# Optimization experiments

Hardware: AMD Instinct MI355X
Metric: run time of the kernel (lower is better)

## Reference

```python
import jax, jax.numpy as jnp
import numpy as np

NEG_SLOPE = 0.2
LN_EPS = 1e-5


def _layernorm(x, g, b):
    mu = jnp.mean(x, axis=-1, keepdims=True)
    var = jnp.mean(jnp.square(x - mu), axis=-1, keepdims=True)
    return (x - mu) * jax.lax.rsqrt(var + LN_EPS) * g + b


def _gat_layer(x, src, dst, ew, W, al, ar, bias, resW, act):
    # x: [N, F_in], W: [F_in, H*D], al/ar: [H, D], bias: [H*D]
    N = x.shape[0]
    H, D = al.shape
    feat = (x @ W).reshape(N, H, D)
    el = jnp.einsum('nhd,hd->nh', feat, al)          # [N, H]
    er = jnp.einsum('nhd,hd->nh', feat, ar)          # [N, H]
    e = jax.nn.leaky_relu(el[src] + er[dst], NEG_SLOPE)  # [E, H]
    # segment softmax over incoming edges of each destination node
    emax = jax.ops.segment_max(e, dst, num_segments=N)
    emax = jnp.where(jnp.isfinite(emax), emax, 0.0)
    ex = jnp.exp(e - emax[dst])
    den = jax.ops.segment_sum(ex, dst, num_segments=N)
    a = ex / den[dst] * ew[:, None]                  # [E, H] (edge_weight scales post-softmax, DGL semantics)
    msg = feat[src] * a[:, :, None]                  # [E, H, D]
    rst = jax.ops.segment_sum(msg, dst, num_segments=N)  # [N, H, D]
    res = (x @ resW).reshape(N, H, D) if resW is not None else x.reshape(N, H, D)
    rst = rst + res + bias.reshape(1, H, D)
    if act is not None:
        rst = act(rst)
    return rst.reshape(N, H * D)


def setup_inputs() -> dict:
    key = jax.random.key(0)
    ks = jax.random.split(key, 24)
    N, E, F_in, H, D = 100000, 1600000, 256, 4, 32
    HD = H * D
    s = 0.1
    inp = {
        'x': jax.random.normal(ks[0], (N, F_in), jnp.float32),
        'src': jax.random.randint(ks[1], (E,), 0, N, jnp.int32),
        'dst': jax.random.randint(ks[2], (E,), 0, N, jnp.int32),
        'edge_weight': jax.random.uniform(ks[3], (E,), jnp.float32),
        # layer 0: in 256 -> 4 heads x 32, residual Linear
        'W0': jax.random.normal(ks[4], (F_in, HD), jnp.float32) * s,
        'al0': jax.random.normal(ks[5], (H, D), jnp.float32) * s,
        'ar0': jax.random.normal(ks[6], (H, D), jnp.float32) * s,
        'b0': jnp.zeros((HD,), jnp.float32),
        'resW0': jax.random.normal(ks[7], (F_in, HD), jnp.float32) * s,
        'ln0_g': jnp.ones((HD,), jnp.float32),
        'ln0_b': jnp.zeros((HD,), jnp.float32),
        # layer 1: 128 -> 4x32, identity residual
        'W1': jax.random.normal(ks[8], (HD, HD), jnp.float32) * s,
        'al1': jax.random.normal(ks[9], (H, D), jnp.float32) * s,
        'ar1': jax.random.normal(ks[10], (H, D), jnp.float32) * s,
        'b1': jnp.zeros((HD,), jnp.float32),
        'ln1_g': jnp.ones((HD,), jnp.float32),
        'ln1_b': jnp.zeros((HD,), jnp.float32),
        # layer 2 (last, no activation)
        'W2': jax.random.normal(ks[11], (HD, HD), jnp.float32) * s,
        'al2': jax.random.normal(ks[12], (H, D), jnp.float32) * s,
        'ar2': jax.random.normal(ks[13], (H, D), jnp.float32) * s,
        'b2': jnp.zeros((HD,), jnp.float32),
        'ln2_g': jnp.ones((HD,), jnp.float32),
        'ln2_b': jnp.zeros((HD,), jnp.float32),
    }
    return inp


def reference(x, src, dst, edge_weight,
              W0, al0, ar0, b0, resW0, ln0_g, ln0_b,
              W1, al1, ar1, b1, ln1_g, ln1_b,
              W2, al2, ar2, b2, ln2_g, ln2_b):
    h = _gat_layer(x, src, dst, edge_weight, W0, al0, ar0, b0, resW0, jax.nn.elu)
    h = _layernorm(h, ln0_g, ln0_b)
    h = _gat_layer(h, src, dst, edge_weight, W1, al1, ar1, b1, None, jax.nn.elu)
    h = _layernorm(h, ln1_g, ln1_b)
    h = _gat_layer(h, src, dst, edge_weight, W2, al2, ar2, b2, None, None)
    h = _layernorm(h, ln2_g, ln2_b)
    return h
```

## Files before the change

kernel.cpp:

```cpp
#include <hip/hip_runtime.h>
#include <hip/hip_bf16.h>
#include <hip/hip_fp16.h>
#include <math.h>

#define DEV __device__ __forceinline__

typedef short v8s __attribute__((ext_vector_type(8)));
typedef float v4f __attribute__((ext_vector_type(4)));
typedef __fp16 fp16x2 __attribute__((ext_vector_type(2)));

DEV float bf2f(unsigned short u) {
    union { unsigned int i; float f; } c; c.i = ((unsigned int)u) << 16; return c.f;
}
DEV unsigned short f2bf(float f) {
    union { float f; unsigned int u; } c; c.f = f;
    unsigned int u = c.u;
    unsigned int r = u + 0x7fffu + ((u >> 16) & 1u);
    return (unsigned short)(r >> 16);
}
DEV unsigned short f2h(float f) {
    union { _Float16 h; unsigned short u; } c; c.h = (_Float16)f; return c.u;
}
DEV float h2f(unsigned short u) {
    union { unsigned short u; _Float16 h; } c; c.u = u; return (float)c.h;
}
DEV unsigned int pkdup(float x) {
    union { fp16x2 h; unsigned int u; } c;
    c.h = __builtin_amdgcn_cvt_pkrtz(x, x);
    return c.u;
}
DEV __half2 bitcast_h2(unsigned int u) {
    union { unsigned int u; __half2 h; } c; c.u = u; return c.h;
}

#if __has_builtin(__builtin_amdgcn_exp2f)
DEV float fexp2(float x) { return __builtin_amdgcn_exp2f(x); }
#else
DEV float fexp2(float x) { float r; asm("v_exp_f32 %0, %1" : "=v"(r) : "v"(x)); return r; }
#endif
#if __has_builtin(__builtin_amdgcn_rcpf)
DEV float frcp(float x) { return __builtin_amdgcn_rcpf(x); }
#else
DEV float frcp(float x) { float r; asm("v_rcp_f32 %0, %1" : "=v"(r) : "v"(x)); return r; }
#endif
#if __has_builtin(__builtin_amdgcn_rsqf)
DEV float frsq(float x) { return __builtin_amdgcn_rsqf(x); }
#else
DEV float frsq(float x) { float r; asm("v_rsq_f32 %0, %1" : "=v"(r) : "v"(x)); return r; }
#endif
DEV unsigned int cvtpk_bf16(float lo, float hi) {
    unsigned int r;
    asm("v_cvt_pk_bf16_f32 %0, %1, %2" : "=v"(r) : "v"(lo), "v"(hi));
    return r;
}

__global__ void detect_kernel(const unsigned short* __restrict__ w, int* __restrict__ flag) {
    __shared__ int cnt;
    if (threadIdx.x == 0) cnt = 0;
    __syncthreads();
    int c = 0;
    for (int i = threadIdx.x; i < 2048; i += 256) {
        unsigned short u = w[i * 2];
        int e = (u >> 7) & 0xff;
        if (e >= 110 && e <= 132) c++;
    }
    atomicAdd(&cnt, c);
    __syncthreads();
    if (threadIdx.x == 0) *flag = (cnt > 1024) ? 1 : 0;
}


__global__ void zero_kernel(int* __restrict__ p, int n) {
    int i = blockIdx.x * 256 + threadIdx.x;
    if (i < n) p[i] = 0;
}

__global__ void degree_kernel(const int* __restrict__ dst, int* __restrict__ deg, int E) {
    int i = blockIdx.x * 256 + threadIdx.x;
    if (i < E) atomicAdd(&deg[dst[i]], 1);
}

__global__ __launch_bounds__(1024)
void scan_kernel(const int* __restrict__ deg, int* __restrict__ rowptr, int n) {
    __shared__ int wtot[16];
    const int tid  = threadIdx.x;
    const int lane = tid & 63;
    const int wid  = tid >> 6;
    int carry = 0;
    for (int base = 0; base < n; base += 4096) {
        int i0 = base + tid * 4;
        int v0 = (i0     < n) ? deg[i0]     : 0;
        int v1 = (i0 + 1 < n) ? deg[i0 + 1] : 0;
        int v2 = (i0 + 2 < n) ? deg[i0 + 2] : 0;
        int v3 = (i0 + 3 < n) ? deg[i0 + 3] : 0;
        int s = v0 + v1 + v2 + v3;
        int sc = s;
        #pragma unroll
        for (int d = 1; d < 64; d <<= 1) {
            int t = __shfl_up(sc, d);
            if (lane >= d) sc += t;
        }
        if (lane == 63) wtot[wid] = sc;
        __syncthreads();
        int woff = 0, tot = 0;
        #pragma unroll
        for (int w = 0; w < 16; ++w) {
            int t = wtot[w];
            if (w < wid) woff += t;
            tot += t;
        }
        int p = carry + woff + (sc - s);
        if (i0     < n) rowptr[i0]     = p; p += v0;
        if (i0 + 1 < n) rowptr[i0 + 1] = p; p += v1;
        if (i0 + 2 < n) rowptr[i0 + 2] = p; p += v2;
        if (i0 + 3 < n) rowptr[i0 + 3] = p;
        carry += tot;
        __syncthreads();
    }
    if (tid == 0) rowptr[n] = carry;
}

__global__ void scatter_kernel(const int* __restrict__ src, const int* __restrict__ dst,
                               const void* __restrict__ ew, const int* __restrict__ flagp,
                               const int* __restrict__ rowptr, int* __restrict__ cur,
                               int2* __restrict__ csr, int E) {
    int i = blockIdx.x * 256 + threadIdx.x;
    if (i < E) {
        int isbf = *flagp;
        int d = dst[i];
        int pos = atomicAdd(&cur[d], 1);
        int slot = rowptr[d] + pos;
        float wv = isbf ? bf2f(((const unsigned short*)ew)[i]) : ((const float*)ew)[i];
        csr[slot] = make_int2(src[i], __float_as_int(wv));
    }
}

__global__ void convx_kernel(const void* __restrict__ x, unsigned short* __restrict__ xbf,
                             const int* __restrict__ flagp, long n8) {
    if (*flagp) return;
    long i = ((long)blockIdx.x * 256 + threadIdx.x) * 8;
    if (i >= n8 * 8) return;
    const float* xf = (const float*)x + i;
    unsigned int o[4];
    #pragma unroll
    for (int j = 0; j < 4; ++j)
        o[j] = cvtpk_bf16(xf[j*2], xf[j*2+1]);
    *(uint4*)(xbf + i) = make_uint4(o[0], o[1], o[2], o[3]);
}

__global__ void wtrans_kernel(const void* __restrict__ B, unsigned short* __restrict__ Btp,
                              const int* __restrict__ flagp, int K) {
    int i = blockIdx.x * 256 + threadIdx.x;
    if (i >= 128 * K) return;
    int j = i & 7;
    int l = (i >> 3) & 63;
    int t = (i >> 9) & 7;
    int c = i >> 12;
    int k = c * 32 + ((l >> 4) * 8) + j;
    int n = t * 16 + (l & 15);
    unsigned short v;
    if (*flagp) v = ((const unsigned short*)B)[k * 128 + n];
    else        v = f2bf(((const float*)B)[k * 128 + n]);
    Btp[i] = v;
}

__global__ __launch_bounds__(256)
void gemm_mfma(const unsigned short* __restrict__ Aext, const unsigned short* __restrict__ Aconv,
               const int* __restrict__ flagp,
               const unsigned short* __restrict__ Btp,
               unsigned short* __restrict__ Cout, int M, int K, int out_half) {
    const unsigned short* A = (*flagp) ? Aext : Aconv;
    const int lane = threadIdx.x & 63;
    const int wid  = threadIdx.x >> 6;
    const long tile = (long)blockIdx.x * 4 + wid;
    const long m0 = tile * 16;
    if (m0 >= M) return;
    const int r = lane & 15, quad = lane >> 4;
    long arow = m0 + r; if (arow >= M) arow = M - 1;
    const unsigned short* ap = A + arow * K + quad * 8;
    v4f acc[8];
    #pragma unroll
    for (int t = 0; t < 8; ++t) acc[t] = (v4f){0.f, 0.f, 0.f, 0.f};
    for (int k0 = 0; k0 < K; k0 += 32) {
        v8s af = *(const v8s*)(ap + k0);
        const unsigned short* bp = Btp + ((size_t)(k0 >> 5) * 8) * 512 + lane * 8;
        #pragma unroll
        for (int t = 0; t < 8; ++t) {
            v8s bf = *(const v8s*)(bp + t * 512);
            acc[t] = __builtin_amdgcn_mfma_f32_16x16x32_bf16(af, bf, acc[t], 0, 0, 0);
        }
    }
    if (out_half) {
        #pragma unroll
        for (int t = 0; t < 8; ++t) {
            const int col = t * 16 + r;
            #pragma unroll
            for (int reg = 0; reg < 4; ++reg) {
                long grow = m0 + quad * 4 + reg;
                if (grow < M) Cout[grow * 128 + col] = f2h(acc[t][reg]);
            }
        }
    } else {
        #pragma unroll
        for (int t = 0; t < 8; t += 2) {
            const int col0 = t * 16 + r, col1 = (t + 1) * 16 + r;
            #pragma unroll
            for (int reg = 0; reg < 4; ++reg) {
                long grow = m0 + quad * 4 + reg;
                unsigned int pk = cvtpk_bf16(acc[t][reg], acc[t + 1][reg]);
                if (grow < M) {
                    Cout[grow * 128 + col0] = (unsigned short)pk;
                    Cout[grow * 128 + col1] = (unsigned short)(pk >> 16);
                }
            }
        }
    }
}

__global__ __launch_bounds__(256)
void elr_kernel(const unsigned short* __restrict__ feath,
                const void* __restrict__ al, const void* __restrict__ ar,
                const int* __restrict__ flagp,
                float* __restrict__ el, float* __restrict__ er, int N) {
    int idx = blockIdx.x * 256 + threadIdx.x;
    if (idx >= N * 4) return;
    const int isbf = *flagp;
    int n = idx >> 2, h = idx & 3;
    const unsigned short* fr = feath + (long)n * 128 + h * 32;
    float av[32], bv[32];
    if (isbf) {
        const unsigned short* alp = (const unsigned short*)al + h * 32;
        const unsigned short* arp = (const unsigned short*)ar + h * 32;
        #pragma unroll
        for (int i = 0; i < 32; ++i) { av[i] = bf2f(alp[i]); bv[i] = bf2f(arp[i]); }
    } else {
        const float* alp = (const float*)al + h * 32;
        const float* arp = (const float*)ar + h * 32;
        #pragma unroll
        for (int i = 0; i < 32; ++i) { av[i] = alp[i]; bv[i] = arp[i]; }
    }
    float sl = 0.f, sr = 0.f;
    #pragma unroll
    for (int i = 0; i < 32; i += 8) {
        uint4 u = *(const uint4*)&fr[i];
        float f[8];
        f[0] = h2f((unsigned short)(u.x & 0xffffu)); f[1] = h2f((unsigned short)(u.x >> 16));
        f[2] = h2f((unsigned short)(u.y & 0xffffu)); f[3] = h2f((unsigned short)(u.y >> 16));
        f[4] = h2f((unsigned short)(u.z & 0xffffu)); f[5] = h2f((unsigned short)(u.z >> 16));
        f[6] = h2f((unsigned short)(u.w & 0xffffu)); f[7] = h2f((unsigned short)(u.w >> 16));
        #pragma unroll
        for (int j = 0; j < 8; ++j) { sl += f[j] * av[i + j]; sr += f[j] * bv[i + j]; }
    }
    el[idx] = sl; er[idx] = sr;
}


__global__ __launch_bounds__(256)
void aggregate_kernel(const unsigned short* __restrict__ feath,
                      const float4* __restrict__ el4,
                      const float4* __restrict__ er4,
                      const unsigned short* __restrict__ res_bf,
                      const void* __restrict__ bias,
                      const void* __restrict__ lng,
                      const void* __restrict__ lnb,
                      const int* __restrict__ flagp,
                      const int* __restrict__ rowptr,
                      const int2* __restrict__ csr,
                      unsigned short* __restrict__ out_bf,
                      float* __restrict__ out_f32,
                      int N, int apply_elu, int final_mode) {
    __shared__ int          s_src[4][64];
    __shared__ unsigned int s_pw[4][256];
    const int lane = threadIdx.x & 63;
    const int wid  = threadIdx.x >> 6;
    const int v = blockIdx.x * 4 + wid;
    if (v >= N) return;
    const int isbf = *flagp;
    const int eg = lane >> 4;
    const int fl = lane & 15;
    const int hd = fl >> 2;
    const int fb = fl * 8;
    const int p0 = rowptr[v], p1 = rowptr[v + 1];
    const float4 erv = er4[v];

    float den0 = 0.f, den1 = 0.f, den2 = 0.f, den3 = 0.f;
    __half2 acch[4];
    acch[0] = acch[1] = acch[2] = acch[3] = __float2half2_rn(0.f);

    for (int eb = p0; eb < p1; eb += 64) {
        const int cnt = min(64, p1 - eb);
        int s = 0;
        unsigned int pw0 = 0, pw1 = 0, pw2 = 0, pw3 = 0;
        if (lane < cnt) {
            int2 sw = csr[eb + lane];
            s = sw.x;
            float w = __int_as_float(sw.y);
            float4 elv = el4[s];
            float t, q;
            t = elv.x + erv.x; t = fmaxf(t, 0.2f * t);
            q = fexp2(fmaf(t, 1.44269504f, -6.0f)); den0 += q; pw0 = pkdup(q * w);
            t = elv.y + erv.y; t = fmaxf(t, 0.2f * t);
            q = fexp2(fmaf(t, 1.44269504f, -6.0f)); den1 += q; pw1 = pkdup(q * w);
            t = elv.z + erv.z; t = fmaxf(t, 0.2f * t);
            q = fexp2(fmaf(t, 1.44269504f, -6.0f)); den2 += q; pw2 = pkdup(q * w);
            t = elv.w + erv.w; t = fmaxf(t, 0.2f * t);
            q = fexp2(fmaf(t, 1.44269504f, -6.0f)); den3 += q; pw3 = pkdup(q * w);
        }
        s_src[wid][lane] = s;
        *(uint4*)&s_pw[wid][lane * 4] = make_uint4(pw0, pw1, pw2, pw3);
        const int cntr = (cnt + 3) & ~3;
        for (int e = 0; e < cntr; e += 4) {
            int ee = e + eg;
            int se = s_src[wid][ee];
            __half2 ae = bitcast_h2(s_pw[wid][ee * 4 + hd]);
            uint4 u = *(const uint4*)(feath + (size_t)se * 128 + fb);
            acch[0] = __hfma2(ae, bitcast_h2(u.x), acch[0]);
            acch[1] = __hfma2(ae, bitcast_h2(u.y), acch[1]);
            acch[2] = __hfma2(ae, bitcast_h2(u.z), acch[2]);
            acch[3] = __hfma2(ae, bitcast_h2(u.w), acch[3]);
        }
    }
    #pragma unroll
    for (int j = 0; j < 4; ++j) {
        union { __half2 h; int i; } a;
        union { int i; __half2 h; } b;
        a.h = acch[j]; b.i = __shfl_xor(a.i, 16); acch[j] = __hadd2(acch[j], b.h);
        a.h = acch[j]; b.i = __shfl_xor(a.i, 32); acch[j] = __hadd2(acch[j], b.h);
    }
    #pragma unroll
    for (int d = 1; d < 64; d <<= 1) {
        den0 += __shfl_xor(den0, d);
        den1 += __shfl_xor(den1, d);
        den2 += __shfl_xor(den2, d);
        den3 += __shfl_xor(den3, d);
    }
    float den = (hd == 0) ? den0 : (hd == 1) ? den1 : (hd == 2) ? den2 : den3;
    float invd = (p1 > p0) ? frcp(den) : 0.f;
    float acc[8];
    #pragma unroll
    for (int j = 0; j < 4; ++j) {
        acc[j * 2]     = __low2float(acch[j]);
        acc[j * 2 + 1] = __high2float(acch[j]);
    }
    uint4 ru = *(const uint4*)(res_bf + (size_t)v * 128 + fb);
    float rv[8];
    rv[0] = bf2f((unsigned short)(ru.x & 0xffffu)); rv[1] = bf2f((unsigned short)(ru.x >> 16));
    rv[2] = bf2f((unsigned short)(ru.y & 0xffffu)); rv[3] = bf2f((unsigned short)(ru.y >> 16));
    rv[4] = bf2f((unsigned short)(ru.z & 0xffffu)); rv[5] = bf2f((unsigned short)(ru.z >> 16));
    rv[6] = bf2f((unsigned short)(ru.w & 0xffffu)); rv[7] = bf2f((unsigned short)(ru.w >> 16));
    float bsv[8], gv[8], lbv[8];
    if (isbf) {
        const unsigned short* bsp = (const unsigned short*)bias + fb;
        const unsigned short* gp  = (const unsigned short*)lng + fb;
        const unsigned short* bp  = (const unsigned short*)lnb + fb;
        #pragma unroll
        for (int j = 0; j < 8; ++j) { bsv[j] = bf2f(bsp[j]); gv[j] = bf2f(gp[j]); lbv[j] = bf2f(bp[j]); }
    } else {
        const float* bsp = (const float*)bias + fb;
        const float* gp  = (const float*)lng + fb;
        const float* bp  = (const float*)lnb + fb;
        #pragma unroll
        for (int j = 0; j < 8; ++j) { bsv[j] = bsp[j]; gv[j] = gp[j]; lbv[j] = bp[j]; }
    }
    float o[8];
    float ssum = 0.f;
    #pragma unroll
    for (int j = 0; j < 8; ++j) {
        float t = acc[j] * invd + rv[j] + bsv[j];
        if (apply_elu) t = (t > 0.f) ? t : fexp2(t * 1.44269504f) - 1.0f;
        o[j] = t;
        ssum += t;
    }
    #pragma unroll
    for (int d = 1; d < 16; d <<= 1) ssum += __shfl_xor(ssum, d);
    float mu = ssum * (1.0f / 128.0f);
    float vsum = 0.f;
    #pragma unroll
    for (int j = 0; j < 8; ++j) { float dd = o[j] - mu; vsum += dd * dd; }
    #pragma unroll
    for (int d = 1; d < 16; d <<= 1) vsum += __shfl_xor(vsum, d);
    float rs = frsq(vsum * (1.0f / 128.0f) + 1e-5f);
    if (eg == 0) {
        if (final_mode && !isbf) {
            float* op = out_f32 + (size_t)v * 128 + fb;
            #pragma unroll
            for (int j = 0; j < 8; ++j) op[j] = (o[j] - mu) * rs * gv[j] + lbv[j];
        } else {
            unsigned int w[4];
            #pragma unroll
            for (int j = 0; j < 4; ++j) {
                float lo = (o[j*2]   - mu) * rs * gv[j*2]   + lbv[j*2];
                float hi = (o[j*2+1] - mu) * rs * gv[j*2+1] + lbv[j*2+1];
                w[j] = cvtpk_bf16(lo, hi);
            }
            *(uint4*)(out_bf + (size_t)v * 128 + fb) = make_uint4(w[0], w[1], w[2], w[3]);
        }
    }
}


extern "C" void kernel_launch(void* const* d_in, const int* in_sizes, int n_in,
                              void* d_out, int out_size, void* d_ws, size_t ws_size,
                              hipStream_t stream) {
    const void* x    = d_in[0];
    const int* src   = (const int*)d_in[1];
    const int* dst   = (const int*)d_in[2];
    const void* ew   = d_in[3];
    const void* W0   = d_in[4];
    const void* al0  = d_in[5];
    const void* ar0  = d_in[6];
    const void* b0   = d_in[7];
    const void* resW0= d_in[8];
    const void* ln0g = d_in[9];
    const void* ln0b = d_in[10];
    const void* W1   = d_in[11];
    const void* al1  = d_in[12];
    const void* ar1  = d_in[13];
    const void* b1   = d_in[14];
    const void* ln1g = d_in[15];
    const void* ln1b = d_in[16];
    const void* W2   = d_in[17];
    const void* al2  = d_in[18];
    const void* ar2  = d_in[19];
    const void* b2   = d_in[20];
    const void* ln2g = d_in[21];
    const void* ln2b = d_in[22];

    const int HD  = 128;
    const int Fin = in_sizes[4] / HD;
    const int N   = in_sizes[0] / Fin;
    const int E   = in_sizes[1];

    char* ws = (char*)d_ws;
    size_t off = 0;
    auto alloc = [&](size_t bytes) -> void* {
        void* p = ws + off;
        off = (off + bytes + 255) & ~(size_t)255;
        return p;
    };
    int*   flag    = (int*)alloc(256);
    unsigned short* xbf   = (unsigned short*)alloc((size_t)N * Fin * 2);
    unsigned short* feat  = (unsigned short*)alloc((size_t)N * 128 * 2);
    unsigned short* h_bf  = (unsigned short*)alloc((size_t)N * 128 * 2);
    unsigned short* res0  = (unsigned short*)alloc((size_t)N * 128 * 2);
    float* el      = (float*)alloc((size_t)N * 4 * 4);
    float* er      = (float*)alloc((size_t)N * 4 * 4);
    int*   rowptr  = (int*)alloc((size_t)(N + 1) * 4);
    int*   deg     = (int*)alloc((size_t)N * 4);
    int*   cur     = (int*)alloc((size_t)N * 4);
    int2*  csr     = (int2*)alloc((size_t)E * 8);
    unsigned short* Bt0  = (unsigned short*)alloc((size_t)128 * Fin * 2);
    unsigned short* Btr0 = (unsigned short*)alloc((size_t)128 * Fin * 2);
    unsigned short* Bt1  = (unsigned short*)alloc((size_t)128 * HD * 2);
    unsigned short* Bt2  = (unsigned short*)alloc((size_t)128 * HD * 2);

    const int zb = (N + 255) / 256;
    const int eb = (E + 255) / 256;
    const int gblocks = (N + 63) / 64;
    const int ablocks = (N + 3) / 4;
    const int lblocks = (N * 4 + 255) / 256;
    const long n8 = (long)N * Fin / 8;
    const int cxb = (int)((n8 + 255) / 256);
    const int wtb0 = (128 * Fin + 255) / 256;
    const int wtb1 = (128 * HD + 255) / 256;

    detect_kernel<<<1, 256, 0, stream>>>((const unsigned short*)W0, flag);

    zero_kernel<<<zb, 256, 0, stream>>>(deg, N);
    zero_kernel<<<zb, 256, 0, stream>>>(cur, N);
    degree_kernel<<<eb, 256, 0, stream>>>(dst, deg, E);
    scan_kernel<<<1, 1024, 0, stream>>>(deg, rowptr, N);
    scatter_kernel<<<eb, 256, 0, stream>>>(src, dst, ew, flag, rowptr, cur, csr, E);

    convx_kernel<<<cxb, 256, 0, stream>>>(x, xbf, flag, n8);
    wtrans_kernel<<<wtb0, 256, 0, stream>>>(W0,    Bt0,  flag, Fin);
    wtrans_kernel<<<wtb0, 256, 0, stream>>>(resW0, Btr0, flag, Fin);
    wtrans_kernel<<<wtb1, 256, 0, stream>>>(W1,    Bt1,  flag, HD);
    wtrans_kernel<<<wtb1, 256, 0, stream>>>(W2,    Bt2,  flag, HD);

    gemm_mfma<<<gblocks, 256, 0, stream>>>((const unsigned short*)x, xbf, flag, Bt0,  feat, N, Fin, 1);
    gemm_mfma<<<gblocks, 256, 0, stream>>>((const unsigned short*)x, xbf, flag, Btr0, res0, N, Fin, 0);
    elr_kernel<<<lblocks, 256, 0, stream>>>(feat, al0, ar0, flag, el, er, N);
    aggregate_kernel<<<ablocks, 256, 0, stream>>>(feat, (const float4*)el, (const float4*)er,
        res0, b0, ln0g, ln0b, flag, rowptr, csr, h_bf, nullptr, N, 1, 0);

    gemm_mfma<<<gblocks, 256, 0, stream>>>(h_bf, h_bf, flag, Bt1, feat, N, HD, 1);
    elr_kernel<<<lblocks, 256, 0, stream>>>(feat, al1, ar1, flag, el, er, N);
    aggregate_kernel<<<ablocks, 256, 0, stream>>>(feat, (const float4*)el, (const float4*)er,
        h_bf, b1, ln1g, ln1b, flag, rowptr, csr, h_bf, nullptr, N, 1, 0);

    gemm_mfma<<<gblocks, 256, 0, stream>>>(h_bf, h_bf, flag, Bt2, feat, N, HD, 1);
    elr_kernel<<<lblocks, 256, 0, stream>>>(feat, al2, ar2, flag, el, er, N);
    aggregate_kernel<<<ablocks, 256, 0, stream>>>(feat, (const float4*)el, (const float4*)er,
        h_bf, b2, ln2g, ln2b, flag, rowptr, csr, (unsigned short*)d_out, (float*)d_out, N, 0, 1);
}
```

Before: 810.2 us.

## Fuse attention logits into GEMM epilogues, merge layer-0 dual GEMM, parallelize scan

The attention score projections (el/er) are now computed in the GEMM epilogue from the fp32 accumulators using cross-lane shuffles, which removes the three separate elr passes that re-read feat. Layer 0 uses one dual GEMM that reads x once, converts fp32 to bf16 inline, and produces both feat and the residual, so the separate convx pass and the second read of x are gone. The single-block CSR row-pointer scan becomes a three-kernel multi-block scan (per-block scan, block-sum scan, offset add). In exchange the fused kernels hold more accumulator registers, which can lower occupancy, and the block-sum scan assumes at most 64 blocks.

```diff
diff --git a/kernel.cpp b/kernel.cpp
--- a/kernel.cpp
+++ b/kernel.cpp
@@ -81,43 +81,58 @@
 }
 
 __global__ __launch_bounds__(1024)
-void scan_kernel(const int* __restrict__ deg, int* __restrict__ rowptr, int n) {
+void pscan_kernel(const int* __restrict__ deg, int* __restrict__ rowptr,
+                  int* __restrict__ bsum, int n) {
     __shared__ int wtot[16];
     const int tid  = threadIdx.x;
     const int lane = tid & 63;
     const int wid  = tid >> 6;
-    int carry = 0;
-    for (int base = 0; base < n; base += 4096) {
-        int i0 = base + tid * 4;
-        int v0 = (i0     < n) ? deg[i0]     : 0;
-        int v1 = (i0 + 1 < n) ? deg[i0 + 1] : 0;
-        int v2 = (i0 + 2 < n) ? deg[i0 + 2] : 0;
-        int v3 = (i0 + 3 < n) ? deg[i0 + 3] : 0;
-        int s = v0 + v1 + v2 + v3;
-        int sc = s;
-        #pragma unroll
-        for (int d = 1; d < 64; d <<= 1) {
-            int t = __shfl_up(sc, d);
-            if (lane >= d) sc += t;
-        }
-        if (lane == 63) wtot[wid] = sc;
-        __syncthreads();
-        int woff = 0, tot = 0;
-        #pragma unroll
-        for (int w = 0; w < 16; ++w) {
-            int t = wtot[w];
-            if (w < wid) woff += t;
-            tot += t;
-        }
-        int p = carry + woff + (sc - s);
-        if (i0     < n) rowptr[i0]     = p; p += v0;
-        if (i0 + 1 < n) rowptr[i0 + 1] = p; p += v1;
-        if (i0 + 2 < n) rowptr[i0 + 2] = p; p += v2;
-        if (i0 + 3 < n) rowptr[i0 + 3] = p;
-        carry += tot;
-        __syncthreads();
-    }
-    if (tid == 0) rowptr[n] = carry;
+    const int i0 = blockIdx.x * 4096 + tid * 4;
+    int v0 = (i0     < n) ? deg[i0]     : 0;
+    int v1 = (i0 + 1 < n) ? deg[i0 + 1] : 0;
+    int v2 = (i0 + 2 < n) ? deg[i0 + 2] : 0;
+    int v3 = (i0 + 3 < n) ? deg[i0 + 3] : 0;
+    int s = v0 + v1 + v2 + v3;
+    int sc = s;
+    #pragma unroll
+    for (int d = 1; d < 64; d <<= 1) {
+        int t = __shfl_up(sc, d);
+        if (lane >= d) sc += t;
+    }
+    if (lane == 63) wtot[wid] = sc;
+    __syncthreads();
+    int woff = 0, tot = 0;
+    #pragma unroll
+    for (int w = 0; w < 16; ++w) {
+        int t = wtot[w];
+        if (w < wid) woff += t;
+        tot += t;
+    }
+    int p = woff + (sc - s);
+    if (i0     < n) rowptr[i0]     = p; p += v0;
+    if (i0 + 1 < n) rowptr[i0 + 1] = p; p += v1;
+    if (i0 + 2 < n) rowptr[i0 + 2] = p; p += v2;
+    if (i0 + 3 < n) rowptr[i0 + 3] = p;
+    if (tid == 0) bsum[blockIdx.x] = tot;
+}
+
+__global__ void bscan_kernel(const int* __restrict__ bsum, int* __restrict__ boff, int nb) {
+    int lane = threadIdx.x & 63;
+    int v = (lane < nb) ? bsum[lane] : 0;
+    int sc = v;
+    #pragma unroll
+    for (int d = 1; d < 64; d <<= 1) {
+        int t = __shfl_up(sc, d);
+        if (lane >= d) sc += t;
+    }
+    if (lane < nb) boff[lane] = sc - v;
+}
+
+__global__ void addoff_kernel(int* __restrict__ rowptr, const int* __restrict__ boff,
+                              int n, int E) {
+    int i = blockIdx.x * 256 + threadIdx.x;
+    if (i < n) rowptr[i] += boff[i >> 12];
+    else if (i == n) rowptr[n] = E;
 }
 
 __global__ void scatter_kernel(const int* __restrict__ src, const int* __restrict__ dst,
@@ -133,19 +148,6 @@
         float wv = isbf ? bf2f(((const unsigned short*)ew)[i]) : ((const float*)ew)[i];
         csr[slot] = make_int2(src[i], __float_as_int(wv));
     }
-}
-
-__global__ void convx_kernel(const void* __restrict__ x, unsigned short* __restrict__ xbf,
-                             const int* __restrict__ flagp, long n8) {
-    if (*flagp) return;
-    long i = ((long)blockIdx.x * 256 + threadIdx.x) * 8;
-    if (i >= n8 * 8) return;
-    const float* xf = (const float*)x + i;
-    unsigned int o[4];
-    #pragma unroll
-    for (int j = 0; j < 4; ++j)
-        o[j] = cvtpk_bf16(xf[j*2], xf[j*2+1]);
-    *(uint4*)(xbf + i) = make_uint4(o[0], o[1], o[2], o[3]);
 }
 
 __global__ void wtrans_kernel(const void* __restrict__ B, unsigned short* __restrict__ Btp,
@@ -164,12 +166,65 @@
     Btp[i] = v;
 }
 
+DEV void elr_epilogue(const v4f* acc, const void* al, const void* ar, int isbf,
+                      int r, int quad, long m0, int M,
+                      float4* el4, float4* er4) {
+    float alv[8], arv[8];
+    if (isbf) {
+        const unsigned short* alp = (const unsigned short*)al;
+        const unsigned short* arp = (const unsigned short*)ar;
+        #pragma unroll
+        for (int h = 0; h < 4; ++h) {
+            alv[2*h]   = bf2f(alp[h*32 + r]);
+            alv[2*h+1] = bf2f(alp[h*32 + 16 + r]);
+            arv[2*h]   = bf2f(arp[h*32 + r]);
+            arv[2*h+1] = bf2f(arp[h*32 + 16 + r]);
+        }
+    } else {
+        const float* alp = (const float*)al;
+        const float* arp = (const float*)ar;
+        #pragma unroll
+        for (int h = 0; h < 4; ++h) {
+            alv[2*h]   = alp[h*32 + r];
+            alv[2*h+1] = alp[h*32 + 16 + r];
+            arv[2*h]   = arp[h*32 + r];
+            arv[2*h+1] = arp[h*32 + 16 + r];
+        }
+    }
+    #pragma unroll
+    for (int reg = 0; reg < 4; ++reg) {
+        float pel[4], per[4];
+        #pragma unroll
+        for (int h = 0; h < 4; ++h) {
+            pel[h] = fmaf(acc[2*h+1][reg], alv[2*h+1], acc[2*h][reg] * alv[2*h]);
+            per[h] = fmaf(acc[2*h+1][reg], arv[2*h+1], acc[2*h][reg] * arv[2*h]);
+        }
+        #pragma unroll
+        for (int d = 1; d < 16; d <<= 1) {
+            #pragma unroll
+            for (int h = 0; h < 4; ++h) {
+                pel[h] += __shfl_xor(pel[h], d);
+                per[h] += __shfl_xor(per[h], d);
+            }
+        }
+        long grow = m0 + quad * 4 + reg;
+        if (grow < M) {
+            if (r == 0) el4[grow] = make_float4(pel[0], pel[1], pel[2], pel[3]);
+            if (r == 1) er4[grow] = make_float4(per[0], per[1], per[2], per[3]);
+        }
+    }
+}
+
 __global__ __launch_bounds__(256)
-void gemm_mfma(const unsigned short* __restrict__ Aext, const unsigned short* __restrict__ Aconv,
-               const int* __restrict__ flagp,
-               const unsigned short* __restrict__ Btp,
-               unsigned short* __restrict__ Cout, int M, int K, int out_half) {
-    const unsigned short* A = (*flagp) ? Aext : Aconv;
+void gemm0_dual(const void* __restrict__ x, const int* __restrict__ flagp,
+                const unsigned short* __restrict__ Bt,
+                const unsigned short* __restrict__ Btr,
+                const void* __restrict__ al, const void* __restrict__ ar,
+                unsigned short* __restrict__ feat,
+                unsigned short* __restrict__ res_bf,
+                float4* __restrict__ el4, float4* __restrict__ er4,
+                int M, int K) {
+    const int isbf = *flagp;
     const int lane = threadIdx.x & 63;
     const int wid  = threadIdx.x >> 6;
     const long tile = (long)blockIdx.x * 4 + wid;
@@ -177,7 +232,84 @@
     if (m0 >= M) return;
     const int r = lane & 15, quad = lane >> 4;
     long arow = m0 + r; if (arow >= M) arow = M - 1;
-    const unsigned short* ap = A + arow * K + quad * 8;
+    v4f accA[8], accB[8];
+    #pragma unroll
+    for (int t = 0; t < 8; ++t) { accA[t] = (v4f){0,0,0,0}; accB[t] = (v4f){0,0,0,0}; }
+    if (isbf) {
+        const unsigned short* ap = (const unsigned short*)x + (size_t)arow * K + quad * 8;
+        for (int k0 = 0; k0 < K; k0 += 32) {
+            v8s af = *(const v8s*)(ap + k0);
+            const unsigned short* bpA = Bt  + ((size_t)(k0 >> 5) * 8) * 512 + lane * 8;
+            const unsigned short* bpB = Btr + ((size_t)(k0 >> 5) * 8) * 512 + lane * 8;
+            #pragma unroll
+            for (int t = 0; t < 8; ++t) {
+                v8s bfA = *(const v8s*)(bpA + t * 512);
+                v8s bfB = *(const v8s*)(bpB + t * 512);
+                accA[t] = __builtin_amdgcn_mfma_f32_16x16x32_bf16(af, bfA, accA[t], 0, 0, 0);
+                accB[t] = __builtin_amdgcn_mfma_f32_16x16x32_bf16(af, bfB, accB[t], 0, 0, 0);
+            }
+        }
+    } else {
+        const float* ap = (const float*)x + (size_t)arow * K + quad * 8;
+        for (int k0 = 0; k0 < K; k0 += 32) {
+            float4 a0 = *(const float4*)(ap + k0);
+            float4 a1 = *(const float4*)(ap + k0 + 4);
+            uint4 u = make_uint4(cvtpk_bf16(a0.x, a0.y), cvtpk_bf16(a0.z, a0.w),
+                                 cvtpk_bf16(a1.x, a1.y), cvtpk_bf16(a1.z, a1.w));
+            union { uint4 u; v8s v; } cc; cc.u = u;
+            v8s af = cc.v;
+            const unsigned short* bpA = Bt  + ((size_t)(k0 >> 5) * 8) * 512 + lane * 8;
+            const unsigned short* bpB = Btr + ((size_t)(k0 >> 5) * 8) * 512 + lane * 8;
+            #pragma unroll
+            for (int t = 0; t < 8; ++t) {
+                v8s bfA = *(const v8s*)(bpA + t * 512);
+                v8s bfB = *(const v8s*)(bpB + t * 512);
+                accA[t] = __builtin_amdgcn_mfma_f32_16x16x32_bf16(af, bfA, accA[t], 0, 0, 0);
+                accB[t] = __builtin_amdgcn_mfma_f32_16x16x32_bf16(af, bfB, accB[t], 0, 0, 0);
+            }
+        }
+    }
+    #pragma unroll
+    for (int t = 0; t < 8; ++t) {
+        const int col = t * 16 + r;
+        #pragma unroll
+        for (int reg = 0; reg < 4; ++reg) {
+            long grow = m0 + quad * 4 + reg;
+            if (grow < M) feat[grow * 128 + col] = f2h(accA[t][reg]);
+        }
+    }
+    #pragma unroll
+    for (int t = 0; t < 8; t += 2) {
+        const int col0 = t * 16 + r, col1 = (t + 1) * 16 + r;
+        #pragma unroll
+        for (int reg = 0; reg < 4; ++reg) {
+            long grow = m0 + quad * 4 + reg;
+            unsigned int pk = cvtpk_bf16(accB[t][reg], accB[t + 1][reg]);
+            if (grow < M) {
+                res_bf[grow * 128 + col0] = (unsigned short)pk;
+                res_bf[grow * 128 + col1] = (unsigned short)(pk >> 16);
+            }
+        }
+    }
+    elr_epilogue(accA, al, ar, isbf, r, quad, m0, M, el4, er4);
+}
+
+__global__ __launch_bounds__(256)
+void gemm_mfma(const unsigned short* __restrict__ A,
+               const unsigned short* __restrict__ Btp,
+               const void* __restrict__ al, const void* __restrict__ ar,
+               const int* __restrict__ flagp,
+               unsigned short* __restrict__ Cout,
+               float4* __restrict__ el4, float4* __restrict__ er4,
+               int M, int K) {
+    const int lane = threadIdx.x & 63;
+    const int wid  = threadIdx.x >> 6;
+    const long tile = (long)blockIdx.x * 4 + wid;
+    const long m0 = tile * 16;
+    if (m0 >= M) return;
+    const int r = lane & 15, quad = lane >> 4;
+    long arow = m0 + r; if (arow >= M) arow = M - 1;
+    const unsigned short* ap = A + (size_t)arow * K + quad * 8;
     v4f acc[8];
     #pragma unroll
     for (int t = 0; t < 8; ++t) acc[t] = (v4f){0.f, 0.f, 0.f, 0.f};
@@ -190,68 +322,16 @@
             acc[t] = __builtin_amdgcn_mfma_f32_16x16x32_bf16(af, bf, acc[t], 0, 0, 0);
         }
     }
-    if (out_half) {
-        #pragma unroll
-        for (int t = 0; t < 8; ++t) {
-            const int col = t * 16 + r;
-            #pragma unroll
-            for (int reg = 0; reg < 4; ++reg) {
-                long grow = m0 + quad * 4 + reg;
-                if (grow < M) Cout[grow * 128 + col] = f2h(acc[t][reg]);
-            }
-        }
-    } else {
-        #pragma unroll
-        for (int t = 0; t < 8; t += 2) {
-            const int col0 = t * 16 + r, col1 = (t + 1) * 16 + r;
-            #pragma unroll
-            for (int reg = 0; reg < 4; ++reg) {
-                long grow = m0 + quad * 4 + reg;
-                unsigned int pk = cvtpk_bf16(acc[t][reg], acc[t + 1][reg]);
-                if (grow < M) {
-                    Cout[grow * 128 + col0] = (unsigned short)pk;
-                    Cout[grow * 128 + col1] = (unsigned short)(pk >> 16);
-                }
-            }
-        }
-    }
-}
-
-__global__ __launch_bounds__(256)
-void elr_kernel(const unsigned short* __restrict__ feath,
-                const void* __restrict__ al, const void* __restrict__ ar,
-                const int* __restrict__ flagp,
-                float* __restrict__ el, float* __restrict__ er, int N) {
-    int idx = blockIdx.x * 256 + threadIdx.x;
-    if (idx >= N * 4) return;
-    const int isbf = *flagp;
-    int n = idx >> 2, h = idx & 3;
-    const unsigned short* fr = feath + (long)n * 128 + h * 32;
-    float av[32], bv[32];
-    if (isbf) {
-        const unsigned short* alp = (const unsigned short*)al + h * 32;
-        const unsigned short* arp = (const unsigned short*)ar + h * 32;
-        #pragma unroll
-        for (int i = 0; i < 32; ++i) { av[i] = bf2f(alp[i]); bv[i] = bf2f(arp[i]); }
-    } else {
-        const float* alp = (const float*)al + h * 32;
-        const float* arp = (const float*)ar + h * 32;
-        #pragma unroll
-        for (int i = 0; i < 32; ++i) { av[i] = alp[i]; bv[i] = arp[i]; }
-    }
-    float sl = 0.f, sr = 0.f;
-    #pragma unroll
-    for (int i = 0; i < 32; i += 8) {
-        uint4 u = *(const uint4*)&fr[i];
-        float f[8];
-        f[0] = h2f((unsigned short)(u.x & 0xffffu)); f[1] = h2f((unsigned short)(u.x >> 16));
-        f[2] = h2f((unsigned short)(u.y & 0xffffu)); f[3] = h2f((unsigned short)(u.y >> 16));
-        f[4] = h2f((unsigned short)(u.z & 0xffffu)); f[5] = h2f((unsigned short)(u.z >> 16));
-        f[6] = h2f((unsigned short)(u.w & 0xffffu)); f[7] = h2f((unsigned short)(u.w >> 16));
-        #pragma unroll
-        for (int j = 0; j < 8; ++j) { sl += f[j] * av[i + j]; sr += f[j] * bv[i + j]; }
-    }
-    el[idx] = sl; er[idx] = sr;
+    #pragma unroll
+    for (int t = 0; t < 8; ++t) {
+        const int col = t * 16 + r;
+        #pragma unroll
+        for (int reg = 0; reg < 4; ++reg) {
+            long grow = m0 + quad * 4 + reg;
+            if (grow < M) Cout[grow * 128 + col] = f2h(acc[t][reg]);
+        }
+    }
+    elr_epilogue(acc, al, ar, *flagp, r, quad, m0, M, el4, er4);
 }
 
 
@@ -439,7 +519,6 @@
         return p;
     };
     int*   flag    = (int*)alloc(256);
-    unsigned short* xbf   = (unsigned short*)alloc((size_t)N * Fin * 2);
     unsigned short* feat  = (unsigned short*)alloc((size_t)N * 128 * 2);
     unsigned short* h_bf  = (unsigned short*)alloc((size_t)N * 128 * 2);
     unsigned short* res0  = (unsigned short*)alloc((size_t)N * 128 * 2);
@@ -448,6 +527,8 @@
     int*   rowptr  = (int*)alloc((size_t)(N + 1) * 4);
     int*   deg     = (int*)alloc((size_t)N * 4);
     int*   cur     = (int*)alloc((size_t)N * 4);
+    int*   bsum    = (int*)alloc(256);
+    int*   boff    = (int*)alloc(256);
     int2*  csr     = (int2*)alloc((size_t)E * 8);
     unsigned short* Bt0  = (unsigned short*)alloc((size_t)128 * Fin * 2);
     unsigned short* Btr0 = (unsigned short*)alloc((size_t)128 * Fin * 2);
@@ -458,9 +539,8 @@
     const int eb = (E + 255) / 256;
     const int gblocks = (N + 63) / 64;
     const int ablocks = (N + 3) / 4;
-    const int lblocks = (N * 4 + 255) / 256;
-    const long n8 = (long)N * Fin / 8;
-    const int cxb = (int)((n8 + 255) / 256);
+    const int nb = (N + 4095) / 4096;
+    const int aob = (N + 1 + 255) / 256;
     const int wtb0 = (128 * Fin + 255) / 256;
     const int wtb1 = (128 * HD + 255) / 256;
 
@@ -469,28 +549,28 @@
     zero_kernel<<<zb, 256, 0, stream>>>(deg, N);
     zero_kernel<<<zb, 256, 0, stream>>>(cur, N);
     degree_kernel<<<eb, 256, 0, stream>>>(dst, deg, E);
-    scan_kernel<<<1, 1024, 0, stream>>>(deg, rowptr, N);
+    pscan_kernel<<<nb, 1024, 0, stream>>>(deg, rowptr, bsum, N);
+    bscan_kernel<<<1, 64, 0, stream>>>(bsum, boff, nb);
+    addoff_kernel<<<aob, 256, 0, stream>>>(rowptr, boff, N, E);
     scatter_kernel<<<eb, 256, 0, stream>>>(src, dst, ew, flag, rowptr, cur, csr, E);
 
-    convx_kernel<<<cxb, 256, 0, stream>>>(x, xbf, flag, n8);
     wtrans_kernel<<<wtb0, 256, 0, stream>>>(W0,    Bt0,  flag, Fin);
     wtrans_kernel<<<wtb0, 256, 0, stream>>>(resW0, Btr0, flag, Fin);
     wtrans_kernel<<<wtb1, 256, 0, stream>>>(W1,    Bt1,  flag, HD);
     wtrans_kernel<<<wtb1, 256, 0, stream>>>(W2,    Bt2,  flag, HD);
 
-    gemm_mfma<<<gblocks, 256, 0, stream>>>((const unsigned short*)x, xbf, flag, Bt0,  feat, N, Fin, 1);
-    gemm_mfma<<<gblocks, 256, 0, stream>>>((const unsigned short*)x, xbf, flag, Btr0, res0, N, Fin, 0);
-    elr_kernel<<<lblocks, 256, 0, stream>>>(feat, al0, ar0, flag, el, er, N);
+    gemm0_dual<<<gblocks, 256, 0, stream>>>(x, flag, Bt0, Btr0, al0, ar0,
+        feat, res0, (float4*)el, (float4*)er, N, Fin);
     aggregate_kernel<<<ablocks, 256, 0, stream>>>(feat, (const float4*)el, (const float4*)er,
         res0, b0, ln0g, ln0b, flag, rowptr, csr, h_bf, nullptr, N, 1, 0);
 
-    gemm_mfma<<<gblocks, 256, 0, stream>>>(h_bf, h_bf, flag, Bt1, feat, N, HD, 1);
-    elr_kernel<<<lblocks, 256, 0, stream>>>(feat, al1, ar1, flag, el, er, N);
+    gemm_mfma<<<gblocks, 256, 0, stream>>>(h_bf, Bt1, al1, ar1, flag, feat,
+        (float4*)el, (float4*)er, N, HD);
     aggregate_kernel<<<ablocks, 256, 0, stream>>>(feat, (const float4*)el, (const float4*)er,
         h_bf, b1, ln1g, ln1b, flag, rowptr, csr, h_bf, nullptr, N, 1, 0);
 
-    gemm_mfma<<<gblocks, 256, 0, stream>>>(h_bf, h_bf, flag, Bt2, feat, N, HD, 1);
-    elr_kernel<<<lblocks, 256, 0, stream>>>(feat, al2, ar2, flag, el, er, N);
+    gemm_mfma<<<gblocks, 256, 0, stream>>>(h_bf, Bt2, al2, ar2, flag, feat,
+        (float4*)el, (float4*)er, N, HD);
     aggregate_kernel<<<ablocks, 256, 0, stream>>>(feat, (const float4*)el, (const float4*)er,
         h_bf, b2, ln2g, ln2b, flag, rowptr, csr, (unsigned short*)d_out, (float*)d_out, N, 0, 1);
 }
```

Result: faster. 722.3 us (-10.9%).
